# Performance work log

Measured on AMD Instinct MI355X. Metric: run time of the kernel, lower is better.

The kernel has to match this reference:

```python
import jax, jax.numpy as jnp
import numpy as np

D = 1024   # hidden_dim
F = 4096   # ffn_dim
E = 8      # expert_num
K = 2      # top_k
B, S = 2, 2048

def setup_inputs() -> dict:
    key = jax.random.key(0)
    ks = jax.random.split(key, 5)
    scale = 0.02
    x = jax.random.normal(ks[0], (B, S, D), dtype=jnp.float32)
    gate_w = jax.random.normal(ks[1], (D, E), dtype=jnp.float32) * scale
    w1 = jax.random.normal(ks[2], (E, D, F), dtype=jnp.float32) * scale
    w3 = jax.random.normal(ks[3], (E, D, F), dtype=jnp.float32) * scale
    w2 = jax.random.normal(ks[4], (E, F, D), dtype=jnp.float32) * scale
    return {"x": x, "gate_w": gate_w, "w1": w1, "w3": w3, "w2": w2}

def reference(x, gate_w, w1, w3, w2):
    # x: [B, S, D] -> tokens [T, D]
    Bb, Ss, Dd = x.shape
    xt = x.reshape(-1, Dd)                                  # [T, D]
    T = xt.shape[0]
    # Router: softmax over experts in float32 (matches torch dtype=torch.float)
    router_probs = jax.nn.softmax((xt @ gate_w).astype(jnp.float32), axis=-1)  # [T, E]
    topk_w, topk_idx = jax.lax.top_k(router_probs, K)        # [T, K]
    topk_w = topk_w / topk_w.sum(axis=-1, keepdims=True)
    topk_w = topk_w.astype(x.dtype)
    # Combine weights scattered to dense [T, E] (equivalent to per-expert gather/scatter loop)
    combine = jnp.zeros((T, E), dtype=x.dtype).at[jnp.arange(T)[:, None], topk_idx].add(topk_w)
    # SwishFFN per expert: w2(silu(x w1) * (x w3)), no bias
    h = jax.nn.silu(jnp.einsum('td,edf->etf', xt, w1)) * jnp.einsum('td,edf->etf', xt, w3)  # [E, T, F]
    out_e = jnp.einsum('etf,efd->etd', h, w2)                # [E, T, D]
    out = jnp.einsum('etd,te->td', out_e, combine)           # [T, D]
    return out.reshape(Bb, Ss, Dd), router_probs
```

## Files before the change

kernel.cpp:

```cpp
#include <hip/hip_runtime.h>

typedef unsigned short u16;
typedef unsigned int u32;
typedef __attribute__((ext_vector_type(8))) short bf16x8;
typedef __attribute__((ext_vector_type(4))) float f32x4;
typedef __attribute__((ext_vector_type(4))) int i32x4;
typedef __attribute__((ext_vector_type(2))) unsigned int u32x2;


__device__ __forceinline__ u16 f2bf(float f) {
  u32 u = __builtin_bit_cast(u32, f);
  u += 0x7fffu + ((u >> 16) & 1u);
  return (u16)(u >> 16);
}
__device__ __forceinline__ u32 pack2(u16 a, u16 b) { return (u32)a | ((u32)b << 16); }

__device__ __forceinline__ char* lds_swz(void* base, int row, int byteInRow) {
  return (char*)base + (((row << 7) + byteInRow) ^ ((row & 7) << 4));
}

#define GLL16(g, l) __builtin_amdgcn_global_load_lds( \
    (const __attribute__((address_space(1))) void*)(g), \
    (__attribute__((address_space(3))) void*)(l), 16, 0, 0)

__global__ __launch_bounds__(256) void prep13_k(
    const float* __restrict__ w1, const float* __restrict__ w3,
    u16* __restrict__ w1t, u16* __restrict__ w3t,
    const float* __restrict__ x, const float* __restrict__ gw,
    float* __restrict__ probs, u16* __restrict__ xb,
    float* __restrict__ wa, int* __restrict__ alist, int* __restrict__ cnt)
{
  __shared__ __align__(16) float smem[16384];
  const int bid = blockIdx.x;
  const int tid = threadIdx.x;
  if (bid >= 4096) {
    const int t0 = bid - 4096;
    const int sel = t0 >> 11;
    const int e   = (t0 >> 8) & 7;
    const int ktb = (t0 >> 4) & 15;
    const int nc  = t0 & 15;
    const float* src = (sel ? w3 : w1) + (size_t)e * 4194304 + (size_t)(ktb * 64) * 4096 + nc * 256;
    u16* dstb = (sel ? w3t : w1t) + (size_t)e * 64 * 16 * 4096 + (size_t)ktb * 4096;

    const int w = tid >> 6, l = tid & 63;
#pragma unroll
    for (int q = 0; q < 16; ++q) {
      const int r = w * 16 + q;
      GLL16(src + (size_t)r * 4096 + l * 4, smem + r * 256);
    }
    asm volatile("s_waitcnt vmcnt(0)" ::: "memory");
    __syncthreads();

    u32 p[32];
#pragma unroll
    for (int i = 0; i < 32; ++i) {
      float a = smem[(2 * i) * 256 + tid];
      float b = smem[(2 * i + 1) * 256 + tid];
      p[i] = pack2(f2bf(a), f2bf(b));
    }
    const int s = tid >> 6, n = tid & 63;
    u16* dp = dstb + (size_t)(nc * 4 + s) * 16 * 4096 + n * 64;
#pragma unroll
    for (int k = 0; k < 8; ++k)
      *(i32x4*)(dp + k * 8) = *(const i32x4*)&p[k * 4];
    return;
  }
  const int t = bid;
  f32x4 xv = ((const f32x4*)(x + (size_t)t * 1024))[tid];
  u32x2 hb;
  hb[0] = pack2(f2bf(xv[0]), f2bf(xv[1]));
  hb[1] = pack2(f2bf(xv[2]), f2bf(xv[3]));
  *(u32x2*)(xb + (size_t)t * 1024 + tid * 4) = hb;

  float acc[8];
#pragma unroll
  for (int e = 0; e < 8; ++e) acc[e] = 0.f;
  const float* g = gw + tid * 32;
#pragma unroll
  for (int j = 0; j < 4; ++j)
#pragma unroll
    for (int e = 0; e < 8; ++e) acc[e] = fmaf(xv[j], g[j * 8 + e], acc[e]);

#pragma unroll
  for (int e = 0; e < 8; ++e)
    for (int off = 32; off > 0; off >>= 1) acc[e] += __shfl_down(acc[e], off);

  float* red = smem;
  const int lane = tid & 63, wid = tid >> 6;
  if (lane == 0) {
#pragma unroll
    for (int e = 0; e < 8; ++e) red[wid * 8 + e] = acc[e];
  }
  __syncthreads();
  if (tid == 0) {
    float p[8]; float mx = -1e30f;
#pragma unroll
    for (int e = 0; e < 8; ++e) { p[e] = red[e] + red[8 + e] + red[16 + e] + red[24 + e]; mx = fmaxf(mx, p[e]); }
    float s = 0.f;
#pragma unroll
    for (int e = 0; e < 8; ++e) { p[e] = __expf(p[e] - mx); s += p[e]; }
    float inv = 1.f / s;
#pragma unroll
    for (int e = 0; e < 8; ++e) { p[e] *= inv; probs[(size_t)t * 8 + e] = p[e]; }
    int i0 = 0;
#pragma unroll
    for (int e = 1; e < 8; ++e) if (p[e] > p[i0]) i0 = e;
    int i1 = (i0 == 0) ? 1 : 0;
#pragma unroll
    for (int e = 0; e < 8; ++e) if (e != i0 && p[e] > p[i1]) i1 = e;
    float s2 = p[i0] + p[i1];
    int pos0 = atomicAdd(&cnt[i0], 1); alist[i0 * 4096 + pos0] = t * 2;
    int pos1 = atomicAdd(&cnt[i1], 1); alist[i1 * 4096 + pos1] = t * 2 + 1;
    wa[t * 2]     = p[i0] / s2;
    wa[t * 2 + 1] = p[i1] / s2;
  }
}

__global__ __launch_bounds__(256, 2) void gemm1w2_k(
    const u16* __restrict__ xb, const u16* __restrict__ w1t, const u16* __restrict__ w3t,
    const int* __restrict__ alist, const int* __restrict__ cnt, u16* __restrict__ H,
    const float* __restrict__ w2, u16* __restrict__ w2t)
{
  __shared__ __align__(16) char smem[33280];
  const int e = blockIdx.z;
  const int bx = blockIdx.x;
  const int tid = threadIdx.x;

  if (bx >= 64) {
    const int slot = ((bx - 64) * 32 + blockIdx.y) * 8 + e;
    const int e2  = slot >> 9;
    const int ktb = (slot >> 3) & 63;
    const int nc  = slot & 7;
    const float* src = w2 + (size_t)e2 * 4194304 + (size_t)(ktb * 64) * 1024 + nc * 128;
    float* lds = (float*)smem;

    const int w = tid >> 6, l = tid & 63;
#pragma unroll
    for (int q = 0; q < 8; ++q) {
      const int r2 = w * 8 + q;
      GLL16(src + (size_t)(2 * r2 + (l >> 5)) * 1024 + (l & 31) * 4, lds + r2 * 256);
    }
    asm volatile("s_waitcnt vmcnt(0)" ::: "memory");
    __syncthreads();

    const int s = (tid >> 6) & 1, n = tid & 63, kh2 = tid >> 7;
    const int cc = s * 64 + n;
    u32 p[16];
#pragma unroll
    for (int i = 0; i < 16; ++i) {
      float a = lds[(kh2 * 32 + 2 * i) * 128 + cc];
      float b = lds[(kh2 * 32 + 2 * i + 1) * 128 + cc];
      p[i] = pack2(f2bf(a), f2bf(b));
    }
    u16* dp = w2t + (((size_t)e2 * 16 + nc * 2 + s) * 64 + ktb) * 4096 + n * 64 + kh2 * 32;
#pragma unroll
    for (int k = 0; k < 4; ++k)
      *(i32x4*)(dp + k * 8) = *(const i32x4*)&p[k * 4];
    return;
  }

  u16* As = (u16*)smem;
  u16* Bs = (u16*)(smem + 16384);
  int* rowid = (int*)(smem + 32768);

  const int mc = cnt[e];
  const int m0 = blockIdx.y * 128;
  if (m0 >= mc) return;
  const int n0 = bx * 64;

  if (tid < 128) rowid[tid] = (m0 + tid < mc) ? alist[e * 4096 + m0 + tid] : -1;
  __syncthreads();

  const int l = tid & 63, w = tid >> 6;
  const u16* wt = (w >> 1) ? w3t : w1t;
  u16* bbase = Bs + (w >> 1) * 4096;

  const u16* aps[4]; const u16* bps[4];
  u16* ald[4]; u16* bld[4];
#pragma unroll
  for (int q = 0; q < 4; ++q) {
    int ra = 32 * w + 8 * q + (l >> 3);
    int id = rowid[ra];
    aps[q] = xb + (size_t)(id < 0 ? 0 : (id >> 1)) * 1024 + ((l & 7) ^ (ra & 7)) * 8;
    ald[q] = As + (32 * w + 8 * q) * 64;
    int rb = 32 * (w & 1) + 8 * q + (l >> 3);
    bps[q] = wt + ((size_t)e * 64 + bx) * 16 * 4096 + rb * 64 + ((l & 7) ^ (rb & 7)) * 8;
    bld[q] = bbase + (32 * (w & 1) + 8 * q) * 64;
  }

  const int wm = (w >> 1) * 64, wn = (w & 1) * 32;
  const int l15 = l & 15, lg = l >> 4;

  f32x4 acc1[4][2], acc3[4][2];
  const f32x4 zf = {0.f, 0.f, 0.f, 0.f};
#pragma unroll
  for (int mi = 0; mi < 4; ++mi) { acc1[mi][0] = zf; acc1[mi][1] = zf; acc3[mi][0] = zf; acc3[mi][1] = zf; }

  for (int kt = 0; kt < 16; ++kt) {
#pragma unroll
    for (int q = 0; q < 4; ++q) GLL16(aps[q] + kt * 64, ald[q]);
#pragma unroll
    for (int q = 0; q < 4; ++q) GLL16(bps[q] + kt * 4096, bld[q]);
    __syncthreads();
#pragma unroll
    for (int ks = 0; ks < 2; ++ks) {
      const int kb = ks * 64 + lg * 16;
      bf16x8 af[4];
#pragma unroll
      for (int mi = 0; mi < 4; ++mi)
        af[mi] = *(const bf16x8*)lds_swz(As, wm + mi * 16 + l15, kb);
#pragma unroll
      for (int ni = 0; ni < 2; ++ni) {
        bf16x8 b1 = *(const bf16x8*)lds_swz(Bs, wn + ni * 16 + l15, kb);
        bf16x8 b3 = *(const bf16x8*)lds_swz(Bs + 4096, wn + ni * 16 + l15, kb);
#pragma unroll
        for (int mi = 0; mi < 4; ++mi) {
          acc1[mi][ni] = __builtin_amdgcn_mfma_f32_16x16x32_bf16(af[mi], b1, acc1[mi][ni], 0, 0, 0);
          acc3[mi][ni] = __builtin_amdgcn_mfma_f32_16x16x32_bf16(af[mi], b3, acc3[mi][ni], 0, 0, 0);
        }
      }
    }
    __syncthreads();
  }

#pragma unroll
  for (int mi = 0; mi < 4; ++mi) {
    const int rb = wm + mi * 16 + lg * 4;
#pragma unroll
    for (int ni = 0; ni < 2; ++ni) {
      const int col = n0 + wn + ni * 16 + l15;
      f32x4 c1 = acc1[mi][ni], c3 = acc3[mi][ni];
#pragma unroll
      for (int j = 0; j < 4; ++j) {
        int id = rowid[rb + j];
        if (id >= 0) {
          float a = c1[j];
          float h = (a / (1.f + __expf(-a))) * c3[j];
          H[(size_t)id * 4096 + col] = f2bf(h);
        }
      }
    }
  }
}

__global__ __launch_bounds__(256, 2) void gemm2_k(
    const u16* __restrict__ H, const u16* __restrict__ w2t,
    const int* __restrict__ alist, const int* __restrict__ cnt,
    const float* __restrict__ wa, float* __restrict__ out)
{
  const int e = blockIdx.z;
  const int mc = cnt[e];
  const int yy = blockIdx.y;
  const int kh = yy & 1;
  const int m0 = (yy >> 1) * 128;
  if (m0 >= mc) return;
  const int n0 = blockIdx.x * 128;
  const int tid = threadIdx.x;

  __shared__ u16 As[128 * 64];
  __shared__ u16 Bs[128 * 64];
  __shared__ int rowid[128];
  __shared__ float rw[128];

  if (tid < 128) {
    int id = (m0 + tid < mc) ? alist[e * 4096 + m0 + tid] : -1;
    rowid[tid] = id;
    rw[tid] = (id >= 0) ? wa[id] : 0.f;
  }
  __syncthreads();

  const int l = tid & 63, w = tid >> 6;
  const size_t kbase = (size_t)kh * 2048;
  const u16* aps[4]; const u16* bps[4];
  u16* ald[4]; u16* bld[4];
#pragma unroll
  for (int q = 0; q < 4; ++q) {
    int ra = 32 * w + 8 * q + (l >> 3);
    int id = rowid[ra];
    aps[q] = H + (size_t)(id < 0 ? 0 : id) * 4096 + kbase + ((l & 7) ^ (ra & 7)) * 8;
    ald[q] = As + (32 * w + 8 * q) * 64;
    int rb = 32 * w + 8 * q + (l >> 3);
    int nt = (n0 >> 6) + (rb >> 6);
    bps[q] = w2t + (((size_t)e * 16 + nt) * 64 + kh * 32) * 4096 + (rb & 63) * 64 + ((l & 7) ^ (rb & 7)) * 8;
    bld[q] = Bs + (32 * w + 8 * q) * 64;
  }

  const int wm = (w >> 1) * 64, wn = (w & 1) * 64;
  const int l15 = l & 15, lg = l >> 4;

  f32x4 acc[4][4];
  const f32x4 zf = {0.f, 0.f, 0.f, 0.f};
#pragma unroll
  for (int mi = 0; mi < 4; ++mi)
#pragma unroll
    for (int ni = 0; ni < 4; ++ni) acc[mi][ni] = zf;

  for (int kt = 0; kt < 32; ++kt) {
#pragma unroll
    for (int q = 0; q < 4; ++q) GLL16(aps[q] + kt * 64, ald[q]);
#pragma unroll
    for (int q = 0; q < 4; ++q) GLL16(bps[q] + kt * 4096, bld[q]);
    __syncthreads();
#pragma unroll
    for (int ks = 0; ks < 2; ++ks) {
      const int kb = ks * 64 + lg * 16;
      bf16x8 af[4];
#pragma unroll
      for (int mi = 0; mi < 4; ++mi)
        af[mi] = *(const bf16x8*)lds_swz(As, wm + mi * 16 + l15, kb);
#pragma unroll
      for (int ni = 0; ni < 4; ++ni) {
        bf16x8 bfb = *(const bf16x8*)lds_swz(Bs, wn + ni * 16 + l15, kb);
#pragma unroll
        for (int mi = 0; mi < 4; ++mi)
          acc[mi][ni] = __builtin_amdgcn_mfma_f32_16x16x32_bf16(af[mi], bfb, acc[mi][ni], 0, 0, 0);
      }
    }
    __syncthreads();
  }

#pragma unroll
  for (int mi = 0; mi < 4; ++mi) {
    const int rb = wm + mi * 16 + lg * 4;
#pragma unroll
    for (int ni = 0; ni < 4; ++ni) {
      const int col = n0 + wn + ni * 16 + l15;
      f32x4 c = acc[mi][ni];
#pragma unroll
      for (int j = 0; j < 4; ++j) {
        int rr = rb + j;
        int id = rowid[rr];
        if (id >= 0)
          unsafeAtomicAdd(&out[(size_t)(id >> 1) * 1024 + col], c[j] * rw[rr]);
      }
    }
  }
}

extern "C" void kernel_launch(void* const* d_in, const int* in_sizes, int n_in,
                              void* d_out, int out_size, void* d_ws, size_t ws_size,
                              hipStream_t stream)
{
  (void)in_sizes; (void)n_in; (void)out_size; (void)ws_size;
  const float* x  = (const float*)d_in[0];
  const float* gw = (const float*)d_in[1];
  const float* w1 = (const float*)d_in[2];
  const float* w3 = (const float*)d_in[3];
  const float* w2 = (const float*)d_in[4];
  float* out   = (float*)d_out;
  float* probs = out + (size_t)4096 * 1024;

  const size_t MB = (size_t)1 << 20;
  char* ws = (char*)d_ws;
  u16*   xb    = (u16*)(ws);
  u16*   H     = (u16*)(ws + 8 * MB);
  u16*   w1t   = (u16*)(ws + 72 * MB);
  u16*   w3t   = (u16*)(ws + 136 * MB);
  u16*   w2t   = (u16*)(ws + 200 * MB);
  float* wa    = (float*)(ws + 264 * MB);
  int*   alist = (int*)(ws + 264 * MB + 32768);
  int*   cnt   = (int*)(ws + 264 * MB + 32768 + 131072);

  hipMemsetAsync(cnt, 0, 8 * sizeof(int), stream);
  hipMemsetAsync(out, 0, (size_t)4096 * 1024 * sizeof(float), stream);
  prep13_k<<<8192, 256, 0, stream>>>(w1, w3, w1t, w3t, x, gw, probs, xb, wa, alist, cnt);
  gemm1w2_k<<<dim3(80, 32, 8), 256, 0, stream>>>(xb, w1t, w3t, alist, cnt, H, w2, w2t);
  gemm2_k<<<dim3(8, 64, 8), 256, 0, stream>>>(H, w2t, alist, cnt, wa, out);
}
```

Baseline: 500.9 us.

## Drop w1/w3 pre-transpose pass; load fp32 weights directly into GEMM1 LDS

Removes the separate pass that converted w1 and w3 to bf16 in a transposed layout, so the prep kernel now only does routing. GEMM1 instead streams the fp32 w1/w3 tiles straight from global memory into LDS and converts them to bf16 fragments at read time with strided LDS loads. This avoids writing and re-reading 128 MB of bf16 weights. In exchange, GEMM1 moves twice as many weight bytes per tile, needs more LDS per block, and adds conversion ALU work and possibly bank-conflicted LDS reads in the inner loop, and every routed M-tile re-reads the fp32 weights.

```diff
diff --git a/kernel.cpp b/kernel.cpp
--- a/kernel.cpp
+++ b/kernel.cpp
@@ -15,6 +15,17 @@
 }
 __device__ __forceinline__ u32 pack2(u16 a, u16 b) { return (u32)a | ((u32)b << 16); }
 
+__device__ __forceinline__ u32 cvt2(float a, float b) { return pack2(f2bf(a), f2bf(b)); }
+
+__device__ __forceinline__ bf16x8 bfrag(const float* bp) {
+  i32x4 v;
+  v[0] = (int)cvt2(bp[0],   bp[64]);
+  v[1] = (int)cvt2(bp[128], bp[192]);
+  v[2] = (int)cvt2(bp[256], bp[320]);
+  v[3] = (int)cvt2(bp[384], bp[448]);
+  return __builtin_bit_cast(bf16x8, v);
+}
+
 __device__ __forceinline__ char* lds_swz(void* base, int row, int byteInRow) {
   return (char*)base + (((row << 7) + byteInRow) ^ ((row & 7) << 4));
 }
@@ -23,49 +34,13 @@
     (const __attribute__((address_space(1))) void*)(g), \
     (__attribute__((address_space(3))) void*)(l), 16, 0, 0)
 
-__global__ __launch_bounds__(256) void prep13_k(
-    const float* __restrict__ w1, const float* __restrict__ w3,
-    u16* __restrict__ w1t, u16* __restrict__ w3t,
+__global__ __launch_bounds__(256) void router_k(
     const float* __restrict__ x, const float* __restrict__ gw,
     float* __restrict__ probs, u16* __restrict__ xb,
     float* __restrict__ wa, int* __restrict__ alist, int* __restrict__ cnt)
 {
-  __shared__ __align__(16) float smem[16384];
-  const int bid = blockIdx.x;
+  const int t = blockIdx.x;
   const int tid = threadIdx.x;
-  if (bid >= 4096) {
-    const int t0 = bid - 4096;
-    const int sel = t0 >> 11;
-    const int e   = (t0 >> 8) & 7;
-    const int ktb = (t0 >> 4) & 15;
-    const int nc  = t0 & 15;
-    const float* src = (sel ? w3 : w1) + (size_t)e * 4194304 + (size_t)(ktb * 64) * 4096 + nc * 256;
-    u16* dstb = (sel ? w3t : w1t) + (size_t)e * 64 * 16 * 4096 + (size_t)ktb * 4096;
-
-    const int w = tid >> 6, l = tid & 63;
-#pragma unroll
-    for (int q = 0; q < 16; ++q) {
-      const int r = w * 16 + q;
-      GLL16(src + (size_t)r * 4096 + l * 4, smem + r * 256);
-    }
-    asm volatile("s_waitcnt vmcnt(0)" ::: "memory");
-    __syncthreads();
-
-    u32 p[32];
-#pragma unroll
-    for (int i = 0; i < 32; ++i) {
-      float a = smem[(2 * i) * 256 + tid];
-      float b = smem[(2 * i + 1) * 256 + tid];
-      p[i] = pack2(f2bf(a), f2bf(b));
-    }
-    const int s = tid >> 6, n = tid & 63;
-    u16* dp = dstb + (size_t)(nc * 4 + s) * 16 * 4096 + n * 64;
-#pragma unroll
-    for (int k = 0; k < 8; ++k)
-      *(i32x4*)(dp + k * 8) = *(const i32x4*)&p[k * 4];
-    return;
-  }
-  const int t = bid;
   f32x4 xv = ((const f32x4*)(x + (size_t)t * 1024))[tid];
   u32x2 hb;
   hb[0] = pack2(f2bf(xv[0]), f2bf(xv[1]));
@@ -85,7 +60,7 @@
   for (int e = 0; e < 8; ++e)
     for (int off = 32; off > 0; off >>= 1) acc[e] += __shfl_down(acc[e], off);
 
-  float* red = smem;
+  __shared__ float red[32];
   const int lane = tid & 63, wid = tid >> 6;
   if (lane == 0) {
 #pragma unroll
@@ -117,11 +92,11 @@
 }
 
 __global__ __launch_bounds__(256, 2) void gemm1w2_k(
-    const u16* __restrict__ xb, const u16* __restrict__ w1t, const u16* __restrict__ w3t,
+    const u16* __restrict__ xb, const float* __restrict__ w1, const float* __restrict__ w3,
     const int* __restrict__ alist, const int* __restrict__ cnt, u16* __restrict__ H,
     const float* __restrict__ w2, u16* __restrict__ w2t)
 {
-  __shared__ __align__(16) char smem[33280];
+  __shared__ __align__(16) char smem[49664];
   const int e = blockIdx.z;
   const int bx = blockIdx.x;
   const int tid = threadIdx.x;
@@ -159,9 +134,9 @@
     return;
   }
 
-  u16* As = (u16*)smem;
-  u16* Bs = (u16*)(smem + 16384);
-  int* rowid = (int*)(smem + 32768);
+  u16*  As   = (u16*)smem;
+  int*  rowid = (int*)(smem + 16384);
+  float* Bs32 = (float*)(smem + 16896);
 
   const int mc = cnt[e];
   const int m0 = blockIdx.y * 128;
@@ -172,24 +147,28 @@
   __syncthreads();
 
   const int l = tid & 63, w = tid >> 6;
-  const u16* wt = (w >> 1) ? w3t : w1t;
-  u16* bbase = Bs + (w >> 1) * 4096;
-
-  const u16* aps[4]; const u16* bps[4];
-  u16* ald[4]; u16* bld[4];
+
+  const u16* aps[4]; u16* ald[4];
 #pragma unroll
   for (int q = 0; q < 4; ++q) {
     int ra = 32 * w + 8 * q + (l >> 3);
     int id = rowid[ra];
     aps[q] = xb + (size_t)(id < 0 ? 0 : (id >> 1)) * 1024 + ((l & 7) ^ (ra & 7)) * 8;
     ald[q] = As + (32 * w + 8 * q) * 64;
-    int rb = 32 * (w & 1) + 8 * q + (l >> 3);
-    bps[q] = wt + ((size_t)e * 64 + bx) * 16 * 4096 + rb * 64 + ((l & 7) ^ (rb & 7)) * 8;
-    bld[q] = bbase + (32 * (w & 1) + 8 * q) * 64;
-  }
+  }
+
+  const float* wsel = (w >> 1) ? w3 : w1;
+  const int kh = w & 1, rl = l >> 4, c0 = l & 15;
+  const float* bsrc = wsel + (size_t)e * 4194304 + (size_t)(kh * 32 + rl) * 4096 + n0;
+  const int ofA = c0 * 4;
+  const int ofB = ((c0 + 4) & 15) * 4;
+  float* bdst = Bs32 + (w >> 1) * 4096 + kh * 2048;
 
   const int wm = (w >> 1) * 64, wn = (w & 1) * 32;
   const int l15 = l & 15, lg = l >> 4;
+  const int gR = lg & 1;
+  const int cp0 = ((wn + l15) + 48 * gR) & 63;
+  const int cp1 = ((wn + 16 + l15) + 48 * gR) & 63;
 
   f32x4 acc1[4][2], acc3[4][2];
   const f32x4 zf = {0.f, 0.f, 0.f, 0.f};
@@ -199,20 +178,25 @@
   for (int kt = 0; kt < 16; ++kt) {
 #pragma unroll
     for (int q = 0; q < 4; ++q) GLL16(aps[q] + kt * 64, ald[q]);
-#pragma unroll
-    for (int q = 0; q < 4; ++q) GLL16(bps[q] + kt * 4096, bld[q]);
-    __syncthreads();
+    const float* bk = bsrc + (size_t)kt * 262144;
+#pragma unroll
+    for (int q = 0; q < 8; ++q)
+      GLL16(bk + q * 16384 + (((q >> 1) & 1) ? ofB : ofA), bdst + q * 256);
+    __syncthreads();
+
 #pragma unroll
     for (int ks = 0; ks < 2; ++ks) {
-      const int kb = ks * 64 + lg * 16;
+      const int kbA = ks * 64 + lg * 16;
       bf16x8 af[4];
 #pragma unroll
       for (int mi = 0; mi < 4; ++mi)
-        af[mi] = *(const bf16x8*)lds_swz(As, wm + mi * 16 + l15, kb);
+        af[mi] = *(const bf16x8*)lds_swz(As, wm + mi * 16 + l15, kbA);
+      const float* b0 = Bs32 + ks * 2048 + lg * 512;
 #pragma unroll
       for (int ni = 0; ni < 2; ++ni) {
-        bf16x8 b1 = *(const bf16x8*)lds_swz(Bs, wn + ni * 16 + l15, kb);
-        bf16x8 b3 = *(const bf16x8*)lds_swz(Bs + 4096, wn + ni * 16 + l15, kb);
+        const int cp = ni ? cp1 : cp0;
+        bf16x8 b1 = bfrag(b0 + cp);
+        bf16x8 b3 = bfrag(b0 + 4096 + cp);
 #pragma unroll
         for (int mi = 0; mi < 4; ++mi) {
           acc1[mi][ni] = __builtin_amdgcn_mfma_f32_16x16x32_bf16(af[mi], b1, acc1[mi][ni], 0, 0, 0);
@@ -354,16 +338,14 @@
   char* ws = (char*)d_ws;
   u16*   xb    = (u16*)(ws);
   u16*   H     = (u16*)(ws + 8 * MB);
-  u16*   w1t   = (u16*)(ws + 72 * MB);
-  u16*   w3t   = (u16*)(ws + 136 * MB);
   u16*   w2t   = (u16*)(ws + 200 * MB);
   float* wa    = (float*)(ws + 264 * MB);
   int*   alist = (int*)(ws + 264 * MB + 32768);
   int*   cnt   = (int*)(ws + 264 * MB + 32768 + 131072);
 
-  hipMemsetAsync(cnt, 0, 8 * sizeof(int), stream);
-  hipMemsetAsync(out, 0, (size_t)4096 * 1024 * sizeof(float), stream);
-  prep13_k<<<8192, 256, 0, stream>>>(w1, w3, w1t, w3t, x, gw, probs, xb, wa, alist, cnt);
-  gemm1w2_k<<<dim3(80, 32, 8), 256, 0, stream>>>(xb, w1t, w3t, alist, cnt, H, w2, w2t);
+  (void)hipMemsetAsync(cnt, 0, 8 * sizeof(int), stream);
+  (void)hipMemsetAsync(out, 0, (size_t)4096 * 1024 * sizeof(float), stream);
+  router_k<<<4096, 256, 0, stream>>>(x, gw, probs, xb, wa, alist, cnt);
+  gemm1w2_k<<<dim3(80, 32, 8), 256, 0, stream>>>(xb, w1, w3, alist, cnt, H, w2, w2t);
   gemm2_k<<<dim3(8, 64, 8), 256, 0, stream>>>(H, w2t, alist, cnt, wa, out);
 }
```

New measurement: 523.7 us. 1.05x slower.
